# Optimization experiments

Measured on AMD Instinct MI355X. Metric: run time of the kernel, lower is better.

Reference implementation:

```python
import jax, jax.numpy as jnp
import numpy as np

# module-level config (mirrors the torch globals)
IMG = (256, 256)
BLK = (8, 8)
N_BLOCKS = 512
N_SEQ = 512
TILES = (IMG[0] // BLK[0]) * (IMG[1] // BLK[1])  # 1024
BATCH = 32
TAU = 0.5


def setup_inputs() -> dict:
    key = jax.random.key(0)
    k1, k2, k3, k4 = jax.random.split(key, 4)
    frame_idxs = jax.random.randint(k1, (BATCH,), 0, N_SEQ)
    sequence = jax.random.normal(k2, (N_SEQ, TILES, N_BLOCKS), jnp.float32)
    blocks = jax.random.normal(k3, (N_BLOCKS, BLK[0], BLK[1]), jnp.float32)
    u = jax.random.uniform(k4, (BATCH, TILES, N_BLOCKS), jnp.float32, 1e-6, 1.0 - 1e-6)
    gumbel = -jnp.log(-jnp.log(u))  # standard Gumbel(0,1) noise
    return {"frame_idxs": frame_idxs, "sequence": sequence, "blocks": blocks, "gumbel": gumbel}


def reference(frame_idxs, sequence, blocks, gumbel):
    # F.gumbel_softmax(logits, tau=0.5, hard=True) with precomputed gumbel noise
    logits = sequence[frame_idxs]                                   # [B, L, N]
    y = jax.nn.softmax((logits + gumbel) / TAU, axis=-1)            # soft sample
    hard = jax.nn.one_hot(jnp.argmax(y, axis=-1), N_BLOCKS, dtype=y.dtype)
    w = hard + y - jax.lax.stop_gradient(y)                         # straight-through

    block_len = BLK[0] * BLK[1]
    # matmul(block_weights, blocks.view(N, block_len)): [B, L, block_len]
    uf = jnp.einsum('bln,nk->blk', w, blocks.reshape(N_BLOCKS, block_len))

    # Fold with stride == kernel_size is a pure reshape/transpose (non-overlapping tiles)
    gh, gw = IMG[0] // BLK[0], IMG[1] // BLK[1]
    img = uf.reshape(BATCH, gh, gw, BLK[0], BLK[1])
    img = img.transpose(0, 1, 3, 2, 4).reshape(BATCH, 1, IMG[0], IMG[1])
    return img
```

## Files before the change

### kernel.cpp

```cpp
#include <hip/hip_runtime.h>
#include <hip/hip_bf16.h>
#include <math.h>

#define IMG_H     256
#define IMG_W     256
#define BLK_H     8
#define BLK_W     8
#define N_BLOCKS  512
#define TILES     1024
#define BATCH     32
#define GRID_W    32

__global__ __launch_bounds__(256) void ImageReconstruction_55825984913931_kernel(
    const int*   __restrict__ frame_idxs,
    const float* __restrict__ sequence,
    const float* __restrict__ blocks,
    const float* __restrict__ gumbel,
    float*       __restrict__ out)
{
    const int wave = threadIdx.x >> 6;
    const int lane = threadIdx.x & 63;
    const int row  = blockIdx.x * 4 + wave;
    const int b    = row >> 10;
    const int l    = row & (TILES - 1);

    const int fi = frame_idxs[b];
    const float* __restrict__ seq_row = sequence + ((size_t)fi * TILES + l) * N_BLOCKS;
    const float* __restrict__ gum_row = gumbel   + ((size_t)b  * TILES + l) * N_BLOCKS;

    float best = -INFINITY;
    int   bidx = 0x7fffffff;

    #pragma unroll
    for (int c = 0; c < 2; ++c) {
        const int base = c * 256 + lane * 4;
        const float4 s = *reinterpret_cast<const float4*>(seq_row + base);
        const float4 g = *reinterpret_cast<const float4*>(gum_row + base);
        const float v[4] = { s.x + g.x, s.y + g.y, s.z + g.z, s.w + g.w };
        #pragma unroll
        for (int j = 0; j < 4; ++j) {
            if (v[j] > best) { best = v[j]; bidx = base + j; }
        }
    }

    #pragma unroll
    for (int off = 32; off >= 1; off >>= 1) {
        const float ov = __shfl_xor(best, off, 64);
        const int   oi = __shfl_xor(bidx, off, 64);
        if (ov > best || (ov == best && oi < bidx)) { best = ov; bidx = oi; }
    }

    const float val = blocks[bidx * (BLK_H * BLK_W) + lane];
    const int ti = l >> 5;
    const int tj = l & (GRID_W - 1);
    const int r  = ti * BLK_H + (lane >> 3);
    const int cc = tj * BLK_W + (lane & 7);
    out[(size_t)b * (IMG_H * IMG_W) + r * IMG_W + cc] = val;
}

extern "C" void kernel_launch(void* const* d_in, const int* in_sizes, int n_in,
                              void* d_out, int out_size, void* d_ws, size_t ws_size,
                              hipStream_t stream) {
    const int*   frame_idxs = (const int*)  d_in[0];
    const float* sequence   = (const float*)d_in[1];
    const float* blocks     = (const float*)d_in[2];
    const float* gumbel     = (const float*)d_in[3];
    float*       out        = (float*)      d_out;

    const int rows = BATCH * TILES;
    const int grid = rows / 4;
    ImageReconstruction_55825984913931_kernel<<<grid, 256, 0, stream>>>(
        frame_idxs, sequence, blocks, gumbel, out);
}
```

Before: 26.08 us.

## Process four rows per wave and stage tiles in LDS for coalesced float4 stores

Each wave now handles four tile rows, issuing all eight vector loads per row up front so more memory requests are in flight before the argmax reductions. The selected 8x8 blocks are written into a shared-memory buffer, and after a barrier the 16 tiles are written out as full 128-byte image-row segments using float4 stores. This replaces the old scattered 32-byte stores per tile and cuts the grid size by four. In exchange it adds register pressure, a __syncthreads, and fewer blocks to hide latency with.

```diff
diff --git a/kernel.cpp b/kernel.cpp
--- a/kernel.cpp
+++ b/kernel.cpp
@@ -4,12 +4,13 @@
 
 #define IMG_H     256
 #define IMG_W     256
-#define BLK_H     8
-#define BLK_W     8
 #define N_BLOCKS  512
 #define TILES     1024
 #define BATCH     32
 #define GRID_W    32
+#define PAD       72
+
+typedef float f32x4 __attribute__((ext_vector_type(4)));
 
 __global__ __launch_bounds__(256) void ImageReconstruction_55825984913931_kernel(
     const int*   __restrict__ frame_idxs,
@@ -18,44 +19,73 @@
     const float* __restrict__ gumbel,
     float*       __restrict__ out)
 {
-    const int wave = threadIdx.x >> 6;
-    const int lane = threadIdx.x & 63;
-    const int row  = blockIdx.x * 4 + wave;
-    const int b    = row >> 10;
-    const int l    = row & (TILES - 1);
+    __shared__ float tilebuf[16][PAD];
 
-    const int fi = frame_idxs[b];
-    const float* __restrict__ seq_row = sequence + ((size_t)fi * TILES + l) * N_BLOCKS;
-    const float* __restrict__ gum_row = gumbel   + ((size_t)b  * TILES + l) * N_BLOCKS;
+    const int wave      = threadIdx.x >> 6;
+    const int lane      = threadIdx.x & 63;
+    const int blockBase = blockIdx.x * 16;
+    const int b         = blockBase >> 10;
+    const int fi        = frame_idxs[b];
+    const int l0        = (blockBase & (TILES - 1)) + wave * 4;
 
-    float best = -INFINITY;
-    int   bidx = 0x7fffffff;
+    const float* __restrict__ seq_base = sequence + ((size_t)fi * TILES + l0) * N_BLOCKS;
+    const float* __restrict__ gum_base = gumbel   + ((size_t)b  * TILES + l0) * N_BLOCKS;
 
+    f32x4 s[4][2], g[4][2];
     #pragma unroll
-    for (int c = 0; c < 2; ++c) {
-        const int base = c * 256 + lane * 4;
-        const float4 s = *reinterpret_cast<const float4*>(seq_row + base);
-        const float4 g = *reinterpret_cast<const float4*>(gum_row + base);
-        const float v[4] = { s.x + g.x, s.y + g.y, s.z + g.z, s.w + g.w };
+    for (int r = 0; r < 4; ++r) {
         #pragma unroll
-        for (int j = 0; j < 4; ++j) {
-            if (v[j] > best) { best = v[j]; bidx = base + j; }
+        for (int c = 0; c < 2; ++c) {
+            const int off = r * N_BLOCKS + c * 256 + lane * 4;
+            s[r][c] = *reinterpret_cast<const f32x4*>(seq_base + off);
+            g[r][c] = *reinterpret_cast<const f32x4*>(gum_base + off);
+        }
+    }
+
+    float best[4]; int bidx[4];
+    #pragma unroll
+    for (int r = 0; r < 4; ++r) {
+        best[r] = -INFINITY; bidx[r] = 0x7fffffff;
+        #pragma unroll
+        for (int c = 0; c < 2; ++c) {
+            const int base = c * 256 + lane * 4;
+            #pragma unroll
+            for (int j = 0; j < 4; ++j) {
+                const float v = s[r][c][j] + g[r][c][j];
+                if (v > best[r]) { best[r] = v; bidx[r] = base + j; }
+            }
         }
     }
 
     #pragma unroll
     for (int off = 32; off >= 1; off >>= 1) {
-        const float ov = __shfl_xor(best, off, 64);
-        const int   oi = __shfl_xor(bidx, off, 64);
-        if (ov > best || (ov == best && oi < bidx)) { best = ov; bidx = oi; }
+        #pragma unroll
+        for (int r = 0; r < 4; ++r) {
+            const float ov = __shfl_xor(best[r], off, 64);
+            const int   oi = __shfl_xor(bidx[r], off, 64);
+            if (ov > best[r] || (ov == best[r] && oi < bidx[r])) {
+                best[r] = ov; bidx[r] = oi;
+            }
+        }
     }
 
-    const float val = blocks[bidx * (BLK_H * BLK_W) + lane];
-    const int ti = l >> 5;
-    const int tj = l & (GRID_W - 1);
-    const int r  = ti * BLK_H + (lane >> 3);
-    const int cc = tj * BLK_W + (lane & 7);
-    out[(size_t)b * (IMG_H * IMG_W) + r * IMG_W + cc] = val;
+    #pragma unroll
+    for (int r = 0; r < 4; ++r)
+        tilebuf[wave * 4 + r][lane] = blocks[bidx[r] * 64 + lane];
+    __syncthreads();
+
+    const int t      = threadIdx.x;
+    const int r_img  = t >> 5;
+    const int c4     = (t & 31) * 4;
+    const int tile   = c4 >> 3;
+    const int within = r_img * 8 + (c4 & 7);
+    const f32x4 v = *reinterpret_cast<const f32x4*>(&tilebuf[tile][within]);
+
+    const int ti  = (blockBase & (TILES - 1)) >> 5;
+    const int tj0 = blockBase & (GRID_W - 1);
+    float* dst = out + (size_t)b * (IMG_H * IMG_W)
+                     + (ti * 8 + r_img) * IMG_W + tj0 * 8 + c4;
+    *reinterpret_cast<f32x4*>(dst) = v;
 }
 
 extern "C" void kernel_launch(void* const* d_in, const int* in_sizes, int n_in,
@@ -67,8 +97,7 @@
     const float* gumbel     = (const float*)d_in[3];
     float*       out        = (float*)      d_out;
 
-    const int rows = BATCH * TILES;
-    const int grid = rows / 4;
+    const int grid = (BATCH * TILES) / 16;
     ImageReconstruction_55825984913931_kernel<<<grid, 256, 0, stream>>>(
         frame_idxs, sequence, blocks, gumbel, out);
 }
```

Result: slower. 28.92 us (+10.9%).
